# Kernel tuning notes

Hardware: AMD Instinct MI355X
Metric: run time of the kernel (lower is better)

Reference implementation:

```python
import jax, jax.numpy as jnp
import numpy as np

N, E = 20000, 640000
LATENT, HID, OUT, HEADS = 512, 256, 128, 2
NEG_SLOPE = 0.2


def setup_inputs() -> dict:
    key = jax.random.key(0)
    ks = jax.random.split(key, 12)
    s = 0.02
    return {
        "z": jax.random.normal(ks[0], (N, LATENT), dtype=jnp.float32),
        "edge_index": jax.random.randint(ks[1], (2, E), 0, N, dtype=jnp.int64),
        "W1": jax.random.normal(ks[2], (LATENT, HID), dtype=jnp.float32) * s,
        "b1": jnp.zeros((HID,), dtype=jnp.float32),
        "W2": jax.random.normal(ks[3], (HID, HID * HEADS), dtype=jnp.float32) * s,
        "b2": jnp.zeros((HID * HEADS,), dtype=jnp.float32),
        "Wg": jax.random.normal(ks[4], (HID * HEADS, HEADS * OUT), dtype=jnp.float32) * s,
        "att_src": jax.random.normal(ks[5], (HEADS, OUT), dtype=jnp.float32) * s,
        "att_dst": jax.random.normal(ks[6], (HEADS, OUT), dtype=jnp.float32) * s,
        "bias_g": jnp.zeros((HEADS * OUT,), dtype=jnp.float32),
        "W3": jax.random.normal(ks[7], (OUT * HEADS, 512), dtype=jnp.float32) * s,
        "b3": jnp.zeros((512,), dtype=jnp.float32),
    }


def _gat_conv(x, edge_index, Wg, att_src, att_dst, bias_g):
    n = x.shape[0]
    # add self loops (PyG GATConv default add_self_loops=True)
    loops = jnp.tile(jnp.arange(n, dtype=edge_index.dtype)[None, :], (2, 1))
    ei = jnp.concatenate([edge_index, loops], axis=1)
    src, dst = ei[0], ei[1]
    xp = (x @ Wg).reshape(n, HEADS, OUT)          # [N,H,C]
    a_src = jnp.einsum('nhc,hc->nh', xp, att_src)  # [N,H]
    a_dst = jnp.einsum('nhc,hc->nh', xp, att_dst)
    alpha = jax.nn.leaky_relu(a_src[src] + a_dst[dst], NEG_SLOPE)  # [E+N,H]
    amax = jax.ops.segment_max(alpha, dst, num_segments=n)
    alpha = jnp.exp(alpha - amax[dst])
    denom = jax.ops.segment_sum(alpha, dst, num_segments=n)
    alpha = alpha / jnp.maximum(denom[dst], 1e-16)
    msg = xp[src] * alpha[:, :, None]              # [E+N,H,C]
    out = jax.ops.segment_sum(msg, dst, num_segments=n)  # [N,H,C]
    return out.reshape(n, HEADS * OUT) + bias_g


def reference(z, edge_index, W1, b1, W2, b2, Wg, att_src, att_dst, bias_g, W3, b3):
    x = jax.nn.relu(z @ W1 + b1)
    x = jax.nn.relu(x @ W2 + b2)
    x = _gat_conv(x, edge_index, Wg, att_src, att_dst, bias_g)
    return x @ W3 + b3
```

## Files before the change

### kernel.cpp

```cpp
#include <hip/hip_runtime.h>
#include <hip/hip_bf16.h>
#include <float.h>

#define N_NODES 20000
#define LATENT  512
#define HID     256
#define OUT_C   128
#define HEADS   2
#define HC      256
#define NEG_SLOPE 0.2f

typedef _Float16 half8 __attribute__((ext_vector_type(8)));
typedef __attribute__((ext_vector_type(4))) float f32x4;

__device__ __forceinline__ ushort f2h(float v) {
    _Float16 h = (_Float16)v;
    return *(ushort*)&h;
}
__device__ __forceinline__ float h2f(ushort u) {
    _Float16 h = *(_Float16*)&u;
    return (float)h;
}

__device__ __forceinline__ void gl_lds16(const ushort* g, ushort* l) {
    __builtin_amdgcn_global_load_lds(
        (const __attribute__((address_space(1))) unsigned int*)g,
        (__attribute__((address_space(3))) unsigned int*)l, 16, 0, 0);
}

template<int BN>
__global__ __launch_bounds__(256) void gemm_f16(
    const ushort* __restrict__ A, const ushort* __restrict__ BT,
    const float* __restrict__ bias,
    float* __restrict__ Cf, ushort* __restrict__ Ch,
    int M, int N, int K, int relu)
{
    static_assert(BN == 64, "vmcnt immediates assume 3 DMAs/chunk");
    constexpr int NI  = BN / 32;
    constexpr int BUF = 4096 + BN * 32;
    __shared__ ushort lds[4 * BUF];

    const int t = threadIdx.x;
    const int l = t & 63;
    const int w = t >> 6;
    const int wm = (w >> 1) * 64;
    const int wn = (w & 1) * (BN / 2);
    const int lm = l & 15;
    const int q  = l >> 4;
    const int q4 = q * 4;

    const int row0 = blockIdx.x * 128;
    const int col0 = blockIdx.y * BN;

    const int jr0 = w * 16 + (l >> 2);
    const int gsh = (((l & 3) ^ ((l >> 4) & 3)) << 3);
    const ushort* gA0 = A + (size_t)(row0 + jr0) * K + gsh;
    const ushort* gA1 = gA0 + (size_t)64 * K;
    const ushort* gB0 = BT + (size_t)(col0 + jr0) * K + gsh;
    const int dA0 = w * 512, dA1 = (4 + w) * 512;
    const int dB0 = 4096 + w * 512;

    const int csw = ((q ^ ((lm >> 2) & 3)) << 3);

    const f32x4 zf = {0.f, 0.f, 0.f, 0.f};
    f32x4 acc[4][NI];
    #pragma unroll
    for (int i = 0; i < 4; ++i)
        #pragma unroll
        for (int j = 0; j < NI; ++j) acc[i][j] = zf;

    const int NC = K >> 5;

    auto issue = [&](int c) {
        ushort* B = lds + (size_t)(c & 3) * BUF;
        const int kk = c * 32;
        gl_lds16(gA0 + kk, B + dA0);
        gl_lds16(gA1 + kk, B + dA1);
        gl_lds16(gB0 + kk, B + dB0);
    };

    auto compute = [&](int c) {
        const ushort* B = lds + (size_t)(c & 3) * BUF;
        half8 bf[NI];
        #pragma unroll
        for (int ni = 0; ni < NI; ++ni) {
            const int boff = (wn + ni * 16 + lm) * 32 + csw;
            bf[ni] = *(const half8*)&B[4096 + boff];
        }
        #pragma unroll
        for (int mi = 0; mi < 4; ++mi) {
            const int aoff = (wm + mi * 16 + lm) * 32 + csw;
            half8 af = *(const half8*)&B[aoff];
            #pragma unroll
            for (int ni = 0; ni < NI; ++ni)
                acc[mi][ni] = __builtin_amdgcn_mfma_f32_16x16x32_f16(
                    af, bf[ni], acc[mi][ni], 0, 0, 0);
        }
    };

    issue(0); issue(1); issue(2);
    for (int c = 0; c < NC; ++c) {
        const int ahead = min(NC - 1 - c, 2);
        if (ahead == 2)      asm volatile("s_waitcnt vmcnt(6)" ::: "memory");
        else if (ahead == 1) asm volatile("s_waitcnt vmcnt(3)" ::: "memory");
        else                 asm volatile("s_waitcnt vmcnt(0)" ::: "memory");
        __builtin_amdgcn_s_barrier();
        __builtin_amdgcn_sched_barrier(0);
        if (c + 3 < NC) issue(c + 3);
        compute(c);
    }

    #pragma unroll
    for (int mi = 0; mi < 4; ++mi) {
        #pragma unroll
        for (int ni = 0; ni < NI; ++ni) {
            const int col = col0 + wn + ni * 16 + lm;
            const float bv = bias ? bias[col] : 0.f;
            #pragma unroll
            for (int r = 0; r < 4; ++r) {
                const int row = row0 + wm + mi * 16 + q4 + r;
                if (row >= M) continue;
                float v = acc[mi][ni][r] + bv;
                if (relu) v = fmaxf(v, 0.f);
                const size_t idx = (size_t)row * N + col;
                if (Cf) Cf[idx] = v;
                if (Ch) Ch[idx] = f2h(v);
            }
        }
    }
}

__global__ __launch_bounds__(256) void cvt_zero_kernel(
    const float* __restrict__ x, ushort* __restrict__ o, int n4,
    int* deg, int* cursor, int n)
{
    int i = blockIdx.x * 256 + threadIdx.x;
    if (i < n) { deg[i] = 0; cursor[i] = 0; }
    if (i >= n4) return;
    float4 v = ((const float4*)x)[i];
    ((ushort4*)o)[i] = make_ushort4(f2h(v.x), f2h(v.y), f2h(v.z), f2h(v.w));
}

__global__ __launch_bounds__(256) void transpose_cvt4_kernel(
    const float* __restrict__ W1, const float* __restrict__ W2,
    const float* __restrict__ Wg, const float* __restrict__ W3,
    ushort* __restrict__ T1, ushort* __restrict__ T2,
    ushort* __restrict__ Tg, ushort* __restrict__ T3)
{
    int idx = blockIdx.x * 256 + threadIdx.x;
    int which = idx >> 17, i = idx & 131071;
    const float* W; ushort* T; int K, N;
    if (which == 0)      { W = W1; T = T1; K = 512; N = 256; }
    else if (which == 1) { W = W2; T = T2; K = 256; N = 512; }
    else if (which == 2) { W = Wg; T = Tg; K = 512; N = 256; }
    else                 { W = W3; T = T3; K = 256; N = 512; }
    int k = i / N, n = i - k * N;
    T[(size_t)n * K + k] = f2h(W[i]);
}

__global__ __launch_bounds__(256) void att_kernel(
    const ushort* __restrict__ xp, const float* __restrict__ att_src,
    const float* __restrict__ att_dst,
    float* __restrict__ a_src, float* __restrict__ a_dst, int n)
{
    int node = (blockIdx.x * 256 + threadIdx.x) >> 6;
    int lane = threadIdx.x & 63;
    if (node >= n) return;
    int h = lane >> 5, lh = lane & 31;
    int c = h * OUT_C + lh * 4;
    const ushort4 v = *(const ushort4*)(xp + (size_t)node * HC + c);
    const float4 as = *(const float4*)(att_src + c);
    const float4 ad = *(const float4*)(att_dst + c);
    float x0 = h2f(v.x), x1 = h2f(v.y), x2 = h2f(v.z), x3 = h2f(v.w);
    float s1 = x0 * as.x + x1 * as.y + x2 * as.z + x3 * as.w;
    float s2 = x0 * ad.x + x1 * ad.y + x2 * ad.z + x3 * ad.w;
    #pragma unroll
    for (int off = 16; off > 0; off >>= 1) {
        s1 += __shfl_xor(s1, off);
        s2 += __shfl_xor(s2, off);
    }
    if (lh == 0) { a_src[2 * node + h] = s1; a_dst[2 * node + h] = s2; }
}

__global__ __launch_bounds__(256) void hist_kernel(
    const int* __restrict__ dst, int* deg, int E_real, int ET)
{
    int e = blockIdx.x * blockDim.x + threadIdx.x;
    if (e >= ET) return;
    int d = (e < E_real) ? dst[e] : (e - E_real);
    atomicAdd(&deg[d], 1);
}

__global__ __launch_bounds__(1024) void scan_kernel(
    const int* __restrict__ deg, int* __restrict__ rowptr, int n)
{
    __shared__ int part[1024];
    const int t = threadIdx.x;
    const int chunk = (n + 1023) / 1024;
    const int lo = t * chunk;
    const int hi = min(lo + chunk, n);
    int s = 0;
    for (int i = lo; i < hi; ++i) s += deg[i];
    part[t] = s;
    __syncthreads();
    #pragma unroll
    for (int off = 1; off < 1024; off <<= 1) {
        int add = (t >= off) ? part[t - off] : 0;
        __syncthreads();
        part[t] += add;
        __syncthreads();
    }
    int run = part[t] - s;
    for (int i = lo; i < hi; ++i) { rowptr[i] = run; run += deg[i]; }
    if (t == 1023) rowptr[n] = part[1023];
}

__global__ __launch_bounds__(256) void scatter_kernel(
    const int* __restrict__ src, const int* __restrict__ dst,
    const int* __restrict__ rowptr, int* cursor,
    int* __restrict__ sorted_src, int E_real, int ET)
{
    int e = blockIdx.x * blockDim.x + threadIdx.x;
    if (e >= ET) return;
    int s, d;
    if (e < E_real) { s = src[e]; d = dst[e]; }
    else            { s = e - E_real; d = s; }
    int pos = rowptr[d] + atomicAdd(&cursor[d], 1);
    sorted_src[pos] = s;
}

__global__ __launch_bounds__(256) void gat_aggregate(
    const int* __restrict__ rowptr, const int* __restrict__ sorted_src,
    const float* __restrict__ a_src, const float* __restrict__ a_dst,
    const ushort* __restrict__ xp, const float* __restrict__ bias_g,
    ushort* __restrict__ xg, int n)
{
    const int d = blockIdx.x * 4 + (threadIdx.x >> 6);
    if (d >= n) return;
    const int lane = threadIdx.x & 63;
    const int hsel = lane & 32;
    const int start = rowptr[d], end = rowptr[d + 1];

    const float ad0 = a_dst[2 * d + 0];
    const float ad1 = a_dst[2 * d + 1];

    float4 acc = make_float4(0.f, 0.f, 0.f, 0.f);
    float denom = 0.f;

    for (int e0 = start; e0 < end; e0 += 32) {
        const int cnt = min(32, end - e0);
        const int idx = lane & 31;
        float wsel = 0.f; int off = 0;
        if (idx < cnt) {
            int s = sorted_src[e0 + idx];
            float v0 = a_src[2 * s + 0] + ad0;
            float v1 = a_src[2 * s + 1] + ad1;
            v0 = (v0 > 0.f) ? v0 : NEG_SLOPE * v0;
            v1 = (v1 > 0.f) ? v1 : NEG_SLOPE * v1;
            wsel = (lane < 32) ? __expf(v0) : __expf(v1);
            off = s * HC;
        }
        int j = 0;
        for (; j + 4 <= cnt; j += 4) {
            float w_[4]; int o_[4];
            #pragma unroll
            for (int u = 0; u < 4; ++u) {
                w_[u] = __shfl(wsel, (j + u) + hsel);
                o_[u] = __shfl(off, j + u);
            }
            ushort4 v_[4];
            #pragma unroll
            for (int u = 0; u < 4; ++u)
                v_[u] = *(const ushort4*)(xp + o_[u] + 4 * lane);
            #pragma unroll
            for (int u = 0; u < 4; ++u) {
                denom += w_[u];
                acc.x += w_[u] * h2f(v_[u].x);
                acc.y += w_[u] * h2f(v_[u].y);
                acc.z += w_[u] * h2f(v_[u].z);
                acc.w += w_[u] * h2f(v_[u].w);
            }
        }
        for (; j < cnt; ++j) {
            const float w = __shfl(wsel, j + hsel);
            const int   o = __shfl(off, j);
            const ushort4 v = *(const ushort4*)(xp + o + 4 * lane);
            denom += w;
            acc.x += w * h2f(v.x); acc.y += w * h2f(v.y);
            acc.z += w * h2f(v.z); acc.w += w * h2f(v.w);
        }
    }

    const float inv = 1.f / fmaxf(denom, 1e-16f);
    const int c = 4 * lane;
    const float4 bg = *(const float4*)(bias_g + c);
    const size_t base = ((size_t)d * HC + c) >> 2;
    ((ushort4*)xg)[base] = make_ushort4(
        f2h(acc.x * inv + bg.x), f2h(acc.y * inv + bg.y),
        f2h(acc.z * inv + bg.z), f2h(acc.w * inv + bg.w));
}

extern "C" void kernel_launch(void* const* d_in, const int* in_sizes, int n_in,
                              void* d_out, int out_size, void* d_ws, size_t ws_size,
                              hipStream_t stream)
{
    const float* z       = (const float*)d_in[0];
    const int*   ei      = (const int*)d_in[1];
    const float* W1      = (const float*)d_in[2];
    const float* b1      = (const float*)d_in[3];
    const float* W2      = (const float*)d_in[4];
    const float* b2      = (const float*)d_in[5];
    const float* Wg      = (const float*)d_in[6];
    const float* att_src = (const float*)d_in[7];
    const float* att_dst = (const float*)d_in[8];
    const float* bias_g  = (const float*)d_in[9];
    const float* W3      = (const float*)d_in[10];
    const float* b3      = (const float*)d_in[11];
    float* out = (float*)d_out;

    const int n = N_NODES;
    const int E_real = in_sizes[1] / 2;
    const int ET = E_real + n;
    const int* src = ei;
    const int* dst = ei + E_real;

    char* p = (char*)d_ws;
    auto alloc = [&](size_t bytes) {
        char* r = p;
        p += (bytes + 63) & ~(size_t)63;
        return r;
    };
    const int np = n + 128;
    ushort* z_f16  = (ushort*)alloc((size_t)np * LATENT * 2);
    ushort* x1_f16 = (ushort*)alloc((size_t)np * HID * 2);
    ushort* xp_f16 = (ushort*)alloc((size_t)n * HC * 2);
    ushort* W1T = (ushort*)alloc((size_t)LATENT * HID * 2);
    ushort* W2T = (ushort*)alloc((size_t)HID * 512 * 2);
    ushort* WgT = (ushort*)alloc((size_t)512 * HC * 2);
    ushort* W3T = (ushort*)alloc((size_t)HC * 512 * 2);
    float* a_src = (float*)alloc((size_t)2 * n * 4);
    float* a_dst = (float*)alloc((size_t)2 * n * 4);
    int* deg        = (int*)alloc((size_t)n * 4);
    int* rowptr     = (int*)alloc(((size_t)n + 1) * 4);
    int* cursor     = (int*)alloc((size_t)n * 4);
    int* sorted_src = (int*)alloc((size_t)ET * 4);
    ushort* x2_f16 = z_f16;
    ushort* xg_f16 = x1_f16;

    const int gm128 = (n + 127) / 128;

    cvt_zero_kernel<<<(n * LATENT / 4 + 255) / 256, 256, 0, stream>>>(
        z, z_f16, n * LATENT / 4, deg, cursor, n);
    transpose_cvt4_kernel<<<(4 * 131072) / 256, 256, 0, stream>>>(
        W1, W2, Wg, W3, W1T, W2T, WgT, W3T);

    gemm_f16<64><<<dim3(gm128, HID / 64), 256, 0, stream>>>(
        z_f16, W1T, b1, nullptr, x1_f16, n, HID, LATENT, 1);
    gemm_f16<64><<<dim3(gm128, 512 / 64), 256, 0, stream>>>(
        x1_f16, W2T, b2, nullptr, x2_f16, n, 512, HID, 1);
    gemm_f16<64><<<dim3(gm128, HC / 64), 256, 0, stream>>>(
        x2_f16, WgT, nullptr, nullptr, xp_f16, n, HC, 512, 0);

    att_kernel<<<(n * 64 + 255) / 256, 256, 0, stream>>>(
        xp_f16, att_src, att_dst, a_src, a_dst, n);
    hist_kernel<<<(ET + 255) / 256, 256, 0, stream>>>(dst, deg, E_real, ET);
    scan_kernel<<<1, 1024, 0, stream>>>(deg, rowptr, n);
    scatter_kernel<<<(ET + 255) / 256, 256, 0, stream>>>(
        src, dst, rowptr, cursor, sorted_src, E_real, ET);
    gat_aggregate<<<(n + 3) / 4, 256, 0, stream>>>(
        rowptr, sorted_src, a_src, a_dst, xp_f16, bias_g, xg_f16, n);

    gemm_f16<64><<<dim3(gm128, 512 / 64), 256, 0, stream>>>(
        xg_f16, W3T, b3, out, nullptr, n, 512, HC, 0);
}
```

Before: 342.2 us.

## Fuse small prologue kernels, merge attention with scan, shrink GEMM pipeline depth

Merges the input conversion and weight transpose into one prologue launch, and moves the degree histogram earlier. Attention-score computation and the row-pointer scan now run as different blocks of one launch. The GEMM drops from a 4-stage to a 3-stage LDS ring with an occupancy hint of 4 blocks per CU, and the aggregation loop unrolls 8 edges instead of 4. The aim is fewer launches and more resident GEMM blocks, at the cost of less prefetch depth and a serial scan block sharing the grid with attention blocks.

```diff
diff --git a/kernel.cpp b/kernel.cpp
--- a/kernel.cpp
+++ b/kernel.cpp
@@ -29,7 +29,7 @@
 }
 
 template<int BN>
-__global__ __launch_bounds__(256) void gemm_f16(
+__global__ __launch_bounds__(256, 4) void gemm_f16(
     const ushort* __restrict__ A, const ushort* __restrict__ BT,
     const float* __restrict__ bias,
     float* __restrict__ Cf, ushort* __restrict__ Ch,
@@ -38,7 +38,7 @@
     static_assert(BN == 64, "vmcnt immediates assume 3 DMAs/chunk");
     constexpr int NI  = BN / 32;
     constexpr int BUF = 4096 + BN * 32;
-    __shared__ ushort lds[4 * BUF];
+    __shared__ ushort lds[3 * BUF];
 
     const int t = threadIdx.x;
     const int l = t & 63;
@@ -72,7 +72,7 @@
     const int NC = K >> 5;
 
     auto issue = [&](int c) {
-        ushort* B = lds + (size_t)(c & 3) * BUF;
+        ushort* B = lds + (size_t)(c % 3) * BUF;
         const int kk = c * 32;
         gl_lds16(gA0 + kk, B + dA0);
         gl_lds16(gA1 + kk, B + dA1);
@@ -80,7 +80,7 @@
     };
 
     auto compute = [&](int c) {
-        const ushort* B = lds + (size_t)(c & 3) * BUF;
+        const ushort* B = lds + (size_t)(c % 3) * BUF;
         half8 bf[NI];
         #pragma unroll
         for (int ni = 0; ni < NI; ++ni) {
@@ -98,15 +98,14 @@
         }
     };
 
-    issue(0); issue(1); issue(2);
+    issue(0); issue(1);
     for (int c = 0; c < NC; ++c) {
-        const int ahead = min(NC - 1 - c, 2);
-        if (ahead == 2)      asm volatile("s_waitcnt vmcnt(6)" ::: "memory");
-        else if (ahead == 1) asm volatile("s_waitcnt vmcnt(3)" ::: "memory");
-        else                 asm volatile("s_waitcnt vmcnt(0)" ::: "memory");
+        __builtin_amdgcn_sched_barrier(0);
+        if (c + 1 < NC) asm volatile("s_waitcnt vmcnt(3)" ::: "memory");
+        else            asm volatile("s_waitcnt vmcnt(0)" ::: "memory");
         __builtin_amdgcn_s_barrier();
         __builtin_amdgcn_sched_barrier(0);
-        if (c + 3 < NC) issue(c + 3);
+        if (c + 2 < NC) issue(c + 2);
         compute(c);
     }
 
@@ -130,56 +129,33 @@
     }
 }
 
-__global__ __launch_bounds__(256) void cvt_zero_kernel(
-    const float* __restrict__ x, ushort* __restrict__ o, int n4,
-    int* deg, int* cursor, int n)
-{
-    int i = blockIdx.x * 256 + threadIdx.x;
-    if (i < n) { deg[i] = 0; cursor[i] = 0; }
-    if (i >= n4) return;
-    float4 v = ((const float4*)x)[i];
-    ((ushort4*)o)[i] = make_ushort4(f2h(v.x), f2h(v.y), f2h(v.z), f2h(v.w));
-}
-
-__global__ __launch_bounds__(256) void transpose_cvt4_kernel(
+#define CVT_BLOCKS 10000
+#define TR_BLOCKS  2048
+__global__ __launch_bounds__(256) void prologue_kernel(
+    const float* __restrict__ z, ushort* __restrict__ z_f16,
+    int* deg, int* cursor, int n,
     const float* __restrict__ W1, const float* __restrict__ W2,
     const float* __restrict__ Wg, const float* __restrict__ W3,
     ushort* __restrict__ T1, ushort* __restrict__ T2,
     ushort* __restrict__ Tg, ushort* __restrict__ T3)
 {
-    int idx = blockIdx.x * 256 + threadIdx.x;
-    int which = idx >> 17, i = idx & 131071;
-    const float* W; ushort* T; int K, N;
-    if (which == 0)      { W = W1; T = T1; K = 512; N = 256; }
-    else if (which == 1) { W = W2; T = T2; K = 256; N = 512; }
-    else if (which == 2) { W = Wg; T = Tg; K = 512; N = 256; }
-    else                 { W = W3; T = T3; K = 256; N = 512; }
-    int k = i / N, n = i - k * N;
-    T[(size_t)n * K + k] = f2h(W[i]);
-}
-
-__global__ __launch_bounds__(256) void att_kernel(
-    const ushort* __restrict__ xp, const float* __restrict__ att_src,
-    const float* __restrict__ att_dst,
-    float* __restrict__ a_src, float* __restrict__ a_dst, int n)
-{
-    int node = (blockIdx.x * 256 + threadIdx.x) >> 6;
-    int lane = threadIdx.x & 63;
-    if (node >= n) return;
-    int h = lane >> 5, lh = lane & 31;
-    int c = h * OUT_C + lh * 4;
-    const ushort4 v = *(const ushort4*)(xp + (size_t)node * HC + c);
-    const float4 as = *(const float4*)(att_src + c);
-    const float4 ad = *(const float4*)(att_dst + c);
-    float x0 = h2f(v.x), x1 = h2f(v.y), x2 = h2f(v.z), x3 = h2f(v.w);
-    float s1 = x0 * as.x + x1 * as.y + x2 * as.z + x3 * as.w;
-    float s2 = x0 * ad.x + x1 * ad.y + x2 * ad.z + x3 * ad.w;
-    #pragma unroll
-    for (int off = 16; off > 0; off >>= 1) {
-        s1 += __shfl_xor(s1, off);
-        s2 += __shfl_xor(s2, off);
-    }
-    if (lh == 0) { a_src[2 * node + h] = s1; a_dst[2 * node + h] = s2; }
+    const int b = blockIdx.x;
+    if (b < CVT_BLOCKS) {
+        int i = b * 256 + threadIdx.x;
+        if (i < n) { deg[i] = 0; cursor[i] = 0; }
+        float4 v = ((const float4*)z)[i];
+        ((ushort4*)z_f16)[i] = make_ushort4(f2h(v.x), f2h(v.y), f2h(v.z), f2h(v.w));
+    } else {
+        int idx = (b - CVT_BLOCKS) * 256 + threadIdx.x;
+        int which = idx >> 17, i = idx & 131071;
+        const float* W; ushort* T; int K, N;
+        if (which == 0)      { W = W1; T = T1; K = 512; N = 256; }
+        else if (which == 1) { W = W2; T = T2; K = 256; N = 512; }
+        else if (which == 2) { W = Wg; T = Tg; K = 512; N = 256; }
+        else                 { W = W3; T = T3; K = 256; N = 512; }
+        int k = i / N, nn = i - k * N;
+        T[(size_t)nn * K + k] = f2h(W[i]);
+    }
 }
 
 __global__ __launch_bounds__(256) void hist_kernel(
@@ -191,28 +167,50 @@
     atomicAdd(&deg[d], 1);
 }
 
-__global__ __launch_bounds__(1024) void scan_kernel(
+__global__ __launch_bounds__(1024) void att_scan_kernel(
+    const ushort* __restrict__ xp, const float* __restrict__ att_src,
+    const float* __restrict__ att_dst,
+    float* __restrict__ a_src, float* __restrict__ a_dst,
     const int* __restrict__ deg, int* __restrict__ rowptr, int n)
 {
     __shared__ int part[1024];
-    const int t = threadIdx.x;
-    const int chunk = (n + 1023) / 1024;
-    const int lo = t * chunk;
-    const int hi = min(lo + chunk, n);
-    int s = 0;
-    for (int i = lo; i < hi; ++i) s += deg[i];
-    part[t] = s;
-    __syncthreads();
-    #pragma unroll
-    for (int off = 1; off < 1024; off <<= 1) {
-        int add = (t >= off) ? part[t - off] : 0;
+    if (blockIdx.x < 1250) {
+        int node = blockIdx.x * 16 + (threadIdx.x >> 6);
+        int lane = threadIdx.x & 63;
+        int h = lane >> 5, lh = lane & 31;
+        int c = h * OUT_C + lh * 4;
+        const ushort4 v = *(const ushort4*)(xp + (size_t)node * HC + c);
+        const float4 as = *(const float4*)(att_src + c);
+        const float4 ad = *(const float4*)(att_dst + c);
+        float x0 = h2f(v.x), x1 = h2f(v.y), x2 = h2f(v.z), x3 = h2f(v.w);
+        float s1 = x0 * as.x + x1 * as.y + x2 * as.z + x3 * as.w;
+        float s2 = x0 * ad.x + x1 * ad.y + x2 * ad.z + x3 * ad.w;
+        #pragma unroll
+        for (int off = 16; off > 0; off >>= 1) {
+            s1 += __shfl_xor(s1, off);
+            s2 += __shfl_xor(s2, off);
+        }
+        if (lh == 0) { a_src[2 * node + h] = s1; a_dst[2 * node + h] = s2; }
+    } else {
+        const int t = threadIdx.x;
+        const int chunk = (n + 1023) / 1024;
+        const int lo = t * chunk;
+        const int hi = min(lo + chunk, n);
+        int s = 0;
+        for (int i = lo; i < hi; ++i) s += deg[i];
+        part[t] = s;
         __syncthreads();
-        part[t] += add;
-        __syncthreads();
-    }
-    int run = part[t] - s;
-    for (int i = lo; i < hi; ++i) { rowptr[i] = run; run += deg[i]; }
-    if (t == 1023) rowptr[n] = part[1023];
+        #pragma unroll
+        for (int off = 1; off < 1024; off <<= 1) {
+            int add = (t >= off) ? part[t - off] : 0;
+            __syncthreads();
+            part[t] += add;
+            __syncthreads();
+        }
+        int run = part[t] - s;
+        for (int i = lo; i < hi; ++i) { rowptr[i] = run; run += deg[i]; }
+        if (t == 1023) rowptr[n] = part[1023];
+    }
 }
 
 __global__ __launch_bounds__(256) void scatter_kernel(
@@ -261,19 +259,19 @@
             off = s * HC;
         }
         int j = 0;
-        for (; j + 4 <= cnt; j += 4) {
-            float w_[4]; int o_[4];
-            #pragma unroll
-            for (int u = 0; u < 4; ++u) {
+        for (; j + 8 <= cnt; j += 8) {
+            float w_[8]; int o_[8];
+            #pragma unroll
+            for (int u = 0; u < 8; ++u) {
                 w_[u] = __shfl(wsel, (j + u) + hsel);
                 o_[u] = __shfl(off, j + u);
             }
-            ushort4 v_[4];
-            #pragma unroll
-            for (int u = 0; u < 4; ++u)
+            ushort4 v_[8];
+            #pragma unroll
+            for (int u = 0; u < 8; ++u)
                 v_[u] = *(const ushort4*)(xp + o_[u] + 4 * lane);
             #pragma unroll
-            for (int u = 0; u < 4; ++u) {
+            for (int u = 0; u < 8; ++u) {
                 denom += w_[u];
                 acc.x += w_[u] * h2f(v_[u].x);
                 acc.y += w_[u] * h2f(v_[u].y);
@@ -349,10 +347,9 @@
 
     const int gm128 = (n + 127) / 128;
 
-    cvt_zero_kernel<<<(n * LATENT / 4 + 255) / 256, 256, 0, stream>>>(
-        z, z_f16, n * LATENT / 4, deg, cursor, n);
-    transpose_cvt4_kernel<<<(4 * 131072) / 256, 256, 0, stream>>>(
-        W1, W2, Wg, W3, W1T, W2T, WgT, W3T);
+    prologue_kernel<<<CVT_BLOCKS + TR_BLOCKS, 256, 0, stream>>>(
+        z, z_f16, deg, cursor, n, W1, W2, Wg, W3, W1T, W2T, WgT, W3T);
+    hist_kernel<<<(ET + 255) / 256, 256, 0, stream>>>(dst, deg, E_real, ET);
 
     gemm_f16<64><<<dim3(gm128, HID / 64), 256, 0, stream>>>(
         z_f16, W1T, b1, nullptr, x1_f16, n, HID, LATENT, 1);
@@ -361,10 +358,8 @@
     gemm_f16<64><<<dim3(gm128, HC / 64), 256, 0, stream>>>(
         x2_f16, WgT, nullptr, nullptr, xp_f16, n, HC, 512, 0);
 
-    att_kernel<<<(n * 64 + 255) / 256, 256, 0, stream>>>(
-        xp_f16, att_src, att_dst, a_src, a_dst, n);
-    hist_kernel<<<(ET + 255) / 256, 256, 0, stream>>>(dst, deg, E_real, ET);
-    scan_kernel<<<1, 1024, 0, stream>>>(deg, rowptr, n);
+    att_scan_kernel<<<1251, 1024, 0, stream>>>(
+        xp_f16, att_src, att_dst, a_src, a_dst, deg, rowptr, n);
     scatter_kernel<<<(ET + 255) / 256, 256, 0, stream>>>(
         src, dst, rowptr, cursor, sorted_src, E_real, ET);
     gat_aggregate<<<(n + 3) / 4, 256, 0, stream>>>(
```

New measurement: 335.4 us. -2.0%, faster.
